# Performance work log

Hardware: AMD Instinct MI355X
Metric: run time of the kernel (lower is better)

## Reference

```python
import jax, jax.numpy as jnp
import numpy as np

N = 100_000      # nodes
E = 1_600_000    # edges
DIN = 128
DH = 128
DOUT = 2
BN_EPS = 1e-5


def setup_inputs() -> dict:
    key = jax.random.key(0)
    ks = jax.random.split(key, 14)
    s_in = 1.0 / np.sqrt(DIN)
    s_h = 1.0 / np.sqrt(DH)
    return {
        "x": jax.random.normal(ks[0], (N, DIN), jnp.float32),
        "edge_index": jax.random.randint(ks[1], (2, E), 0, N, jnp.int32),
        "W1": jax.random.normal(ks[2], (DIN, DH), jnp.float32) * s_in,
        "b1": jnp.zeros((DH,), jnp.float32),
        "W2": jax.random.normal(ks[3], (DH, DH), jnp.float32) * s_h,
        "b2": jnp.zeros((DH,), jnp.float32),
        "W3": jax.random.normal(ks[4], (DH, DH), jnp.float32) * s_h,
        "b3": jnp.zeros((DH,), jnp.float32),
        "gamma": jnp.ones((DH,), jnp.float32),
        "beta": jnp.zeros((DH,), jnp.float32),
        "Wc": jax.random.normal(ks[5], (DH, DH), jnp.float32) * s_h,
        "bc": jnp.zeros((DH,), jnp.float32),
        "Wr": jax.random.normal(ks[6], (DH, DOUT), jnp.float32) * s_h,
        "br": jnp.zeros((DOUT,), jnp.float32),
    }


def reference(x, edge_index, W1, b1, W2, b2, W3, b3, gamma, beta, Wc, bc, Wr, br):
    src, dst = edge_index[0], edge_index[1]
    # GCN symmetric normalization with self-loops (deg includes self-loop)
    deg = jnp.zeros((N,), x.dtype).at[dst].add(1.0) + 1.0
    dinv = jax.lax.rsqrt(deg)
    coef = (dinv[src] * dinv[dst])[:, None]        # [E,1]
    self_coef = (dinv * dinv)[:, None]             # [N,1] self-loop weight

    def gcn_conv(h, W, b):
        h = h @ W                                  # [N,DH] dense transform
        agg = jnp.zeros((N, h.shape[1]), h.dtype).at[dst].add(h[src] * coef)
        return agg + h * self_coef + b

    h = jax.nn.relu(gcn_conv(x, W1, b1))
    h = jax.nn.relu(gcn_conv(h, W2, b2))   # dropout is identity at inference
    h = jax.nn.relu(gcn_conv(h, W3, b3))
    # BatchNorm1d over the node dimension (training-mode batch statistics)
    mu = h.mean(axis=0)
    var = h.var(axis=0)
    h = (h - mu) * jax.lax.rsqrt(var + BN_EPS) * gamma + beta
    h = jax.nn.relu(h @ Wc + bc)
    return h @ Wr + br
```

## Files before the change

kernel.cpp:

```cpp
#include <hip/hip_runtime.h>

#define DHC 128
#define BSHIFT 8
#define BSIZE 256

typedef __attribute__((ext_vector_type(8))) __bf16 bf16x8;
typedef __attribute__((ext_vector_type(8))) unsigned short ushort8;
typedef __attribute__((ext_vector_type(4))) float floatx4;

__device__ inline unsigned short f2bf(float f) {
    unsigned int u = __float_as_uint(f);
    return (unsigned short)((u + 0x7FFFu + ((u >> 16) & 1u)) >> 16);
}
__device__ inline float bf2f_lo(unsigned int v) { return __uint_as_float(v << 16); }
__device__ inline float bf2f_hi(unsigned int v) { return __uint_as_float(v & 0xFFFF0000u); }


__global__ __launch_bounds__(256) void bucket_hist(const int* __restrict__ dst,
                                                   int* __restrict__ bcount, int e) {
    __shared__ int h[512];
    for (int i = threadIdx.x; i < 512; i += 256) h[i] = 0;
    __syncthreads();
    int base = blockIdx.x * 4096 + threadIdx.x;
#pragma unroll
    for (int j = 0; j < 16; j++) {
        int i = base + j * 256;
        if (i < e) atomicAdd(&h[dst[i] >> BSHIFT], 1);
    }
    __syncthreads();
    for (int i = threadIdx.x; i < 512; i += 256)
        if (h[i]) atomicAdd(&bcount[i], h[i]);
}

__global__ void bucket_scan(const int* __restrict__ bcount, int* __restrict__ bbase,
                            int* __restrict__ bcur, int nb, int e) {
    __shared__ int s[512];
    int t = threadIdx.x;
    s[t] = (t < nb) ? bcount[t] : 0;
    __syncthreads();
    for (int off = 1; off < 512; off <<= 1) {
        int add = (t >= off) ? s[t - off] : 0;
        __syncthreads();
        s[t] += add;
        __syncthreads();
    }
    if (t < nb) {
        int ex = (t == 0) ? 0 : s[t - 1];
        bbase[t] = ex;
        bcur[t] = ex;
    }
    if (t == 0) bbase[nb] = e;
}

__global__ __launch_bounds__(256) void bucket_scatter(const int* __restrict__ src,
                                                      const int* __restrict__ dst,
                                                      int* __restrict__ bcur,
                                                      unsigned int* __restrict__ ebuf, int e) {
    __shared__ int h[512];
    __shared__ int rsv[512];
    for (int i = threadIdx.x; i < 512; i += 256) h[i] = 0;
    __syncthreads();
    int base = blockIdx.x * 4096 + threadIdx.x;
    int sreg[16], dreg[16];
#pragma unroll
    for (int j = 0; j < 16; j++) {
        int i = base + j * 256;
        if (i < e) {
            sreg[j] = src[i];
            dreg[j] = dst[i];
            atomicAdd(&h[dreg[j] >> BSHIFT], 1);
        } else {
            dreg[j] = -1;
        }
    }
    __syncthreads();
    for (int i = threadIdx.x; i < 512; i += 256) {
        int c = h[i];
        rsv[i] = c ? atomicAdd(&bcur[i], c) : 0;
        h[i] = 0;
    }
    __syncthreads();
#pragma unroll
    for (int j = 0; j < 16; j++) {
        if (dreg[j] >= 0) {
            int b = dreg[j] >> BSHIFT;
            int pos = rsv[b] + atomicAdd(&h[b], 1);
            ebuf[pos] = (unsigned int)sreg[j] | ((unsigned int)(dreg[j] & (BSIZE - 1)) << 20);
        }
    }
}

__global__ __launch_bounds__(256) void bucket_dega(const unsigned int* __restrict__ ebuf,
                                                   const int* __restrict__ bbase,
                                                   int* __restrict__ degs,
                                                   int* __restrict__ pbsum,
                                                   float* __restrict__ dinv, int n) {
    __shared__ int ldeg[256];
    __shared__ int red[256];
    int b = blockIdx.x, t = threadIdx.x;
    int beg = bbase[b], end = bbase[b + 1];
    ldeg[t] = 0;
    __syncthreads();
    for (int i = beg + t; i < end; i += 256) atomicAdd(&ldeg[ebuf[i] >> 20], 1);
    __syncthreads();
    int node = (b << BSHIFT) + t;
    int deg = ldeg[t];
    int pdeg = (deg + 7) & ~7;
    if (node < n) {
        degs[node] = deg;
        dinv[node] = rsqrtf((float)(deg + 1));
    } else {
        pdeg = 0;
    }
    red[t] = pdeg;
    __syncthreads();
    for (int off = 128; off > 0; off >>= 1) {
        if (t < off) red[t] += red[t + off];
        __syncthreads();
    }
    if (t == 0) pbsum[b] = red[0];
}

__global__ void pscan(const int* __restrict__ pbsum, int* __restrict__ pbase,
                      int* __restrict__ row_ptr, int nb, int n) {
    __shared__ int s[512];
    int t = threadIdx.x;
    s[t] = (t < nb) ? pbsum[t] : 0;
    __syncthreads();
    for (int off = 1; off < 512; off <<= 1) {
        int add = (t >= off) ? s[t - off] : 0;
        __syncthreads();
        s[t] += add;
        __syncthreads();
    }
    if (t < nb) pbase[t] = (t == 0) ? 0 : s[t - 1];
    if (t == 0) {
        pbase[nb] = s[nb - 1];
        row_ptr[n] = s[nb - 1];
    }
}

__global__ __launch_bounds__(256) void bucket_csr(const unsigned int* __restrict__ ebuf,
                                                  const int* __restrict__ bbase,
                                                  const int* __restrict__ pbase,
                                                  const int* __restrict__ degs,
                                                  int* __restrict__ row_ptr,
                                                  int* __restrict__ csr, int n) {
    __shared__ int lcur[256];
    __shared__ int lscan[256];
    int b = blockIdx.x, t = threadIdx.x;
    int beg = bbase[b], end = bbase[b + 1];
    int node = (b << BSHIFT) + t;
    int deg = (node < n) ? degs[node] : 0;
    int pdeg = (deg + 7) & ~7;
    lscan[t] = pdeg;
    __syncthreads();
    for (int off = 1; off < 256; off <<= 1) {
        int add = (t >= off) ? lscan[t - off] : 0;
        __syncthreads();
        lscan[t] += add;
        __syncthreads();
    }
    int rp = pbase[b] + lscan[t] - pdeg;
    if (node < n) row_ptr[node] = rp;
    lcur[t] = rp;
    __syncthreads();
    for (int i = beg + t; i < end; i += 256) {
        unsigned int p = ebuf[i];
        int pos = atomicAdd(&lcur[p >> 20], 1);
        csr[pos] = (int)(p & 0xFFFFFu);
    }
    __syncthreads();
    for (int j = deg; j < pdeg; j++) csr[rp + j] = n;
}

__global__ void wconv3_k(const float* __restrict__ W1, const float* __restrict__ W2,
                         const float* __restrict__ W3, unsigned short* __restrict__ WTall,
                         unsigned short* __restrict__ dumA, unsigned short* __restrict__ dumB) {
    if (blockIdx.x == 0 && threadIdx.x < 128) {
        dumA[threadIdx.x] = 0;
        dumB[threadIdx.x] = 0;
    }
    int idx = blockIdx.x * 256 + threadIdx.x;
    int wsel = idx >> 14;
    int i = idx & 16383;
    int nn = i >> 7, k = i & 127;
    const float* W = (wsel == 0) ? W1 : (wsel == 1) ? W2 : W3;
    WTall[idx] = f2bf(W[k * 128 + nn]);
}

template <int MODE, int AF32>
__global__ __launch_bounds__(256, 4) void gemm_k(const void* __restrict__ Avoid,
                                                 const unsigned short* __restrict__ WT,
                                                 const float* __restrict__ bias,
                                                 unsigned short* __restrict__ outB,
                                                 float* __restrict__ outF,
                                                 const float* __restrict__ Wr,
                                                 const float* __restrict__ br,
                                                 const float* __restrict__ dinvp, int n) {
    __shared__ unsigned short Ws[32 * 512];
    {
        for (int c = threadIdx.x; c < 2048; c += 256) {
            int f = c >> 6;
            int l = c & 63;
            int ks = f >> 3, ct = f & 7;
            int nn = ct * 16 + (l & 15);
            int kb = ks * 32 + (l >> 4) * 8;
            *(uint4*)(&Ws[c * 8]) = *(const uint4*)(&WT[nn * 128 + kb]);
        }
    }
    __syncthreads();
    const int wave = threadIdx.x >> 6;
    const int lane = threadIdx.x & 63;
    const int rowbase = blockIdx.x * 128 + wave * 32;
    const int m = lane & 15;
    const int kq = lane >> 4;

    floatx4 acc[2][8];
#pragma unroll
    for (int rt = 0; rt < 2; rt++)
#pragma unroll
        for (int ct = 0; ct < 8; ct++) acc[rt][ct] = (floatx4){0.f, 0.f, 0.f, 0.f};

    const int r0 = min(rowbase + m, n - 1);
    const int r1 = min(rowbase + 16 + m, n - 1);

#pragma unroll
    for (int ks = 0; ks < 4; ks++) {
        const int kb = ks * 32 + kq * 8;
        bf16x8 a0, a1;
        if (AF32) {
            const float* Af = (const float*)Avoid;
            float4 f00 = *(const float4*)(Af + (size_t)r0 * 128 + kb);
            float4 f01 = *(const float4*)(Af + (size_t)r0 * 128 + kb + 4);
            float4 f10 = *(const float4*)(Af + (size_t)r1 * 128 + kb);
            float4 f11 = *(const float4*)(Af + (size_t)r1 * 128 + kb + 4);
            ushort8 u0, u1;
            u0[0] = f2bf(f00.x); u0[1] = f2bf(f00.y); u0[2] = f2bf(f00.z); u0[3] = f2bf(f00.w);
            u0[4] = f2bf(f01.x); u0[5] = f2bf(f01.y); u0[6] = f2bf(f01.z); u0[7] = f2bf(f01.w);
            u1[0] = f2bf(f10.x); u1[1] = f2bf(f10.y); u1[2] = f2bf(f10.z); u1[3] = f2bf(f10.w);
            u1[4] = f2bf(f11.x); u1[5] = f2bf(f11.y); u1[6] = f2bf(f11.z); u1[7] = f2bf(f11.w);
            a0 = __builtin_bit_cast(bf16x8, u0);
            a1 = __builtin_bit_cast(bf16x8, u1);
        } else {
            const unsigned short* Ab = (const unsigned short*)Avoid;
            a0 = __builtin_bit_cast(bf16x8, *(const ushort8*)(Ab + (size_t)r0 * 128 + kb));
            a1 = __builtin_bit_cast(bf16x8, *(const ushort8*)(Ab + (size_t)r1 * 128 + kb));
        }
#pragma unroll
        for (int ct = 0; ct < 8; ct++) {
            bf16x8 bfr = __builtin_bit_cast(bf16x8,
                *(const ushort8*)(&Ws[(ks * 8 + ct) * 512 + lane * 8]));
            acc[0][ct] = __builtin_amdgcn_mfma_f32_16x16x32_bf16(a0, bfr, acc[0][ct], 0, 0, 0);
            acc[1][ct] = __builtin_amdgcn_mfma_f32_16x16x32_bf16(a1, bfr, acc[1][ct], 0, 0, 0);
        }
    }

    if (MODE == 0) {
#pragma unroll
        for (int rt = 0; rt < 2; rt++) {
#pragma unroll
            for (int i = 0; i < 4; i++) {
                int r = rowbase + rt * 16 + kq * 4 + i;
                if (r < n) {
                    float dv = dinvp[r];
#pragma unroll
                    for (int ct = 0; ct < 8; ct++) {
                        int col = ct * 16 + m;
                        outB[(size_t)r * 128 + col] = f2bf(acc[rt][ct][i] * dv);
                    }
                }
            }
        }
    } else {
        float bcv[8], wr0[8], wr1[8];
#pragma unroll
        for (int ct = 0; ct < 8; ct++) {
            int col = ct * 16 + m;
            bcv[ct] = bias[col];
            float2 wv = ((const float2*)Wr)[col];
            wr0[ct] = wv.x;
            wr1[ct] = wv.y;
        }
        float br0 = br[0], br1 = br[1];
#pragma unroll
        for (int rt = 0; rt < 2; rt++) {
#pragma unroll
            for (int i = 0; i < 4; i++) {
                float p0 = 0.f, p1 = 0.f;
#pragma unroll
                for (int ct = 0; ct < 8; ct++) {
                    float v = fmaxf(acc[rt][ct][i] + bcv[ct], 0.f);
                    p0 = fmaf(v, wr0[ct], p0);
                    p1 = fmaf(v, wr1[ct], p1);
                }
#pragma unroll
                for (int mk = 1; mk < 16; mk <<= 1) {
                    p0 += __shfl_xor(p0, mk);
                    p1 += __shfl_xor(p1, mk);
                }
                int r = rowbase + rt * 16 + kq * 4 + i;
                if (m == 0 && r < n) ((float2*)outF)[r] = make_float2(p0 + br0, p1 + br1);
            }
        }
    }
}

#define ACC8(v)                                          \
    a[0] += bf2f_lo((v).x); a[1] += bf2f_hi((v).x);      \
    a[2] += bf2f_lo((v).y); a[3] += bf2f_hi((v).y);      \
    a[4] += bf2f_lo((v).z); a[5] += bf2f_hi((v).z);      \
    a[6] += bf2f_lo((v).w); a[7] += bf2f_hi((v).w);

__global__ __launch_bounds__(256) void agg_k(const unsigned short* __restrict__ hS,
                                             const int* __restrict__ csr,
                                             const int* __restrict__ row_ptr,
                                             const float* __restrict__ dinv,
                                             const float* __restrict__ bias,
                                             unsigned short* __restrict__ out, int n) {
    int node = blockIdx.x * 16 + (threadIdx.x >> 4);
    int t = threadIdx.x & 15;
    if (node >= n) return;
    const uint4* h4 = (const uint4*)hS;
    uint4 vs = h4[(size_t)node * 16 + t];
    int beg = row_ptr[node], pend = row_ptr[node + 1];
    float dd = dinv[node];

    float a[8];
    a[0] = bf2f_lo(vs.x); a[1] = bf2f_hi(vs.x);
    a[2] = bf2f_lo(vs.y); a[3] = bf2f_hi(vs.y);
    a[4] = bf2f_lo(vs.z); a[5] = bf2f_hi(vs.z);
    a[6] = bf2f_lo(vs.w); a[7] = bf2f_hi(vs.w);

    const int4* cp = (const int4*)(csr + beg);
    int nc = (pend - beg) >> 3;
    if (nc > 0) {
        int4 i0 = cp[0], i1 = cp[1];
        for (int k = 0; k < nc; k++) {
            uint4 v0 = h4[(size_t)(unsigned)i0.x * 16 + t];
            uint4 v1 = h4[(size_t)(unsigned)i0.y * 16 + t];
            uint4 v2 = h4[(size_t)(unsigned)i0.z * 16 + t];
            uint4 v3 = h4[(size_t)(unsigned)i0.w * 16 + t];
            uint4 v4 = h4[(size_t)(unsigned)i1.x * 16 + t];
            uint4 v5 = h4[(size_t)(unsigned)i1.y * 16 + t];
            uint4 v6 = h4[(size_t)(unsigned)i1.z * 16 + t];
            uint4 v7 = h4[(size_t)(unsigned)i1.w * 16 + t];
            int4 p0 = cp[2 * k + 2];
            int4 p1 = cp[2 * k + 3];
            ACC8(v0); ACC8(v1); ACC8(v2); ACC8(v3);
            ACC8(v4); ACC8(v5); ACC8(v6); ACC8(v7);
            i0 = p0; i1 = p1;
        }
    }

    float4 b0 = ((const float4*)bias)[t * 2];
    float4 b1 = ((const float4*)bias)[t * 2 + 1];
    uint4 o;
    o.x = (unsigned int)f2bf(fmaxf(fmaf(dd, a[0], b0.x), 0.f)) |
          ((unsigned int)f2bf(fmaxf(fmaf(dd, a[1], b0.y), 0.f)) << 16);
    o.y = (unsigned int)f2bf(fmaxf(fmaf(dd, a[2], b0.z), 0.f)) |
          ((unsigned int)f2bf(fmaxf(fmaf(dd, a[3], b0.w), 0.f)) << 16);
    o.z = (unsigned int)f2bf(fmaxf(fmaf(dd, a[4], b1.x), 0.f)) |
          ((unsigned int)f2bf(fmaxf(fmaf(dd, a[5], b1.y), 0.f)) << 16);
    o.w = (unsigned int)f2bf(fmaxf(fmaf(dd, a[6], b1.z), 0.f)) |
          ((unsigned int)f2bf(fmaxf(fmaf(dd, a[7], b1.w), 0.f)) << 16);
    ((uint4*)out)[(size_t)node * 16 + t] = o;
}

__global__ __launch_bounds__(256) void bn_stats(const unsigned short* __restrict__ h,
                                                float* __restrict__ gsum,
                                                float* __restrict__ gsumsq, int n) {
    __shared__ float red[4][256];
    int l = threadIdx.x & 63;
    int rs = threadIdx.x >> 6;
    float s0 = 0.f, s1 = 0.f, q0 = 0.f, q1 = 0.f;
    for (int r = blockIdx.x * 4 + rs; r < n; r += gridDim.x * 4) {
        unsigned int v = *(const unsigned int*)(h + (size_t)r * 128 + l * 2);
        float a = bf2f_lo(v), b = bf2f_hi(v);
        s0 += a;
        s1 += b;
        q0 = fmaf(a, a, q0);
        q1 = fmaf(b, b, q1);
    }
    red[0][threadIdx.x] = s0;
    red[1][threadIdx.x] = s1;
    red[2][threadIdx.x] = q0;
    red[3][threadIdx.x] = q1;
    __syncthreads();
    if (threadIdx.x < 64) {
        float S0 = 0.f, S1 = 0.f, Q0 = 0.f, Q1 = 0.f;
#pragma unroll
        for (int j = 0; j < 4; j++) {
            S0 += red[0][j * 64 + l];
            S1 += red[1][j * 64 + l];
            Q0 += red[2][j * 64 + l];
            Q1 += red[3][j * 64 + l];
        }
        atomicAdd(&gsum[2 * l + 0], S0);
        atomicAdd(&gsum[2 * l + 1], S1);
        atomicAdd(&gsumsq[2 * l + 0], Q0);
        atomicAdd(&gsumsq[2 * l + 1], Q1);
    }
}

__global__ void bn_finalize(const float* __restrict__ gsum, const float* __restrict__ gsumsq,
                            const float* __restrict__ gamma, const float* __restrict__ beta,
                            const float* __restrict__ bc, float* __restrict__ scale,
                            float* __restrict__ shift, float* __restrict__ bcP, float invN) {
    int j = threadIdx.x;
    float mu = gsum[j] * invN;
    float var = gsumsq[j] * invN - mu * mu;
    float sc = gamma[j] * rsqrtf(var + 1e-5f);
    scale[j] = sc;
    shift[j] = beta[j] - mu * sc;
    bcP[j] = bc[j];
}

__global__ __launch_bounds__(256) void wcfold(const float* __restrict__ Wc,
                                              const float* __restrict__ scale,
                                              const float* __restrict__ shift,
                                              unsigned short* __restrict__ WcT,
                                              float* __restrict__ bcP) {
    __shared__ float scS[128], shS[128];
    if (threadIdx.x < 128) {
        scS[threadIdx.x] = scale[threadIdx.x];
        shS[threadIdx.x] = shift[threadIdx.x];
    }
    __syncthreads();
    int idx = blockIdx.x * 256 + threadIdx.x;
    int j = idx & 127, k = idx >> 7;
    float w = Wc[k * 128 + j];
    WcT[j * 128 + k] = f2bf(scS[k] * w);
    atomicAdd(&bcP[j], shS[k] * w);
}


extern "C" void kernel_launch(void* const* d_in, const int* in_sizes, int n_in,
                              void* d_out, int out_size, void* d_ws, size_t ws_size,
                              hipStream_t stream) {
    const float* x = (const float*)d_in[0];
    const int* ei = (const int*)d_in[1];
    const float* W1 = (const float*)d_in[2];
    const float* b1 = (const float*)d_in[3];
    const float* W2 = (const float*)d_in[4];
    const float* b2 = (const float*)d_in[5];
    const float* W3 = (const float*)d_in[6];
    const float* b3 = (const float*)d_in[7];
    const float* gamma = (const float*)d_in[8];
    const float* beta = (const float*)d_in[9];
    const float* Wc = (const float*)d_in[10];
    const float* bc = (const float*)d_in[11];
    const float* Wr = (const float*)d_in[12];
    const float* br = (const float*)d_in[13];
    float* out = (float*)d_out;

    const int N = in_sizes[0] / DHC;
    const int E = in_sizes[1] / 2;
    const int* srcIdx = ei;
    const int* dstIdx = ei + E;
    const int NB = (N + BSIZE - 1) >> BSHIFT;

    char* w = (char*)d_ws;
    size_t off = 0;
    auto alloc = [&](size_t bytes) -> void* {
        void* p = w + off;
        off += (bytes + 255) & ~(size_t)255;
        return p;
    };
    unsigned short* bufA = (unsigned short*)alloc((size_t)(N + 1) * DHC * 2);
    unsigned short* bufB = (unsigned short*)alloc((size_t)(N + 1) * DHC * 2);
    unsigned int* ebuf = (unsigned int*)alloc((size_t)E * 4);
    int* csr_src = (int*)alloc(((size_t)E + 8 * (size_t)N + 16) * 4);
    int* row_ptr = (int*)alloc((size_t)(N + 1) * 4);
    float* dinv = (float*)alloc((size_t)N * 4);
    int* degs = (int*)alloc((size_t)N * 4);
    int* bcount = (int*)alloc(512 * 4 + 256 * 4);
    float* stats = (float*)(bcount + 512);
    float* gsum = stats;
    float* gsumsq = stats + 128;
    int* bbase = (int*)alloc(513 * 4);
    int* bcur = (int*)alloc(512 * 4);
    int* pbsum = (int*)alloc(512 * 4);
    int* pbase = (int*)alloc(513 * 4);
    unsigned short* WTall = (unsigned short*)alloc((size_t)3 * 16384 * 2);
    unsigned short* WT1 = WTall;
    unsigned short* WT2 = WTall + 16384;
    unsigned short* WT3 = WTall + 32768;
    unsigned short* WcT = (unsigned short*)alloc(16384 * 2);
    float* scale = (float*)alloc(128 * 4);
    float* shift = (float*)alloc(128 * 4);
    float* bcP = (float*)alloc(128 * 4);
    (void)ws_size; (void)n_in; (void)out_size;

    hipMemsetAsync(bcount, 0, 512 * 4 + 256 * 4, stream);

    const int EB = (E + 4095) / 4096;
    bucket_hist<<<EB, 256, 0, stream>>>(dstIdx, bcount, E);
    bucket_scan<<<1, 512, 0, stream>>>(bcount, bbase, bcur, NB, E);
    bucket_scatter<<<EB, 256, 0, stream>>>(srcIdx, dstIdx, bcur, ebuf, E);
    bucket_dega<<<NB, 256, 0, stream>>>(ebuf, bbase, degs, pbsum, dinv, N);
    pscan<<<1, 512, 0, stream>>>(pbsum, pbase, row_ptr, NB, N);
    bucket_csr<<<NB, 256, 0, stream>>>(ebuf, bbase, pbase, degs, row_ptr, csr_src, N);

    wconv3_k<<<192, 256, 0, stream>>>(W1, W2, W3, WTall,
                                      bufA + (size_t)N * DHC, bufB + (size_t)N * DHC);

    const int gemmBlocks = (N + 127) / 128;
    const int aggBlocks = (N + 15) / 16;

    gemm_k<0, 1><<<gemmBlocks, 256, 0, stream>>>(x, WT1, nullptr, bufB, nullptr, nullptr, nullptr, dinv, N);
    agg_k<<<aggBlocks, 256, 0, stream>>>(bufB, csr_src, row_ptr, dinv, b1, bufA, N);
    gemm_k<0, 0><<<gemmBlocks, 256, 0, stream>>>(bufA, WT2, nullptr, bufB, nullptr, nullptr, nullptr, dinv, N);
    agg_k<<<aggBlocks, 256, 0, stream>>>(bufB, csr_src, row_ptr, dinv, b2, bufA, N);
    gemm_k<0, 0><<<gemmBlocks, 256, 0, stream>>>(bufA, WT3, nullptr, bufB, nullptr, nullptr, nullptr, dinv, N);
    agg_k<<<aggBlocks, 256, 0, stream>>>(bufB, csr_src, row_ptr, dinv, b3, bufA, N);

    bn_stats<<<256, 256, 0, stream>>>(bufA, gsum, gsumsq, N);
    bn_finalize<<<1, 128, 0, stream>>>(gsum, gsumsq, gamma, beta, bc, scale, shift, bcP, 1.0f / (float)N);
    wcfold<<<64, 256, 0, stream>>>(Wc, scale, shift, WcT, bcP);
    gemm_k<2, 0><<<gemmBlocks, 256, 0, stream>>>(bufA, WcT, bcP, nullptr, out, Wr, br, dinv, N);
}
```

Measured before the change: 449.9 us.

## Split aggregation into feature halves and fuse BN statistics into last aggregation

The aggregation kernel now processes one 64-feature half per launch, with 8 threads per node and 32 nodes per block, and is launched twice per layer. Each launch gathers half as many bytes per neighbor row, which shrinks the working set so gathered rows are more likely to hit in L2/MALL. The last layer's aggregation also accumulates BatchNorm sums and sums of squares through shuffles, shared atomics and global atomics, removing the separate bn_stats pass. The costs are that CSR indices and row pointers are read twice per layer and there are extra launches.

```diff
diff --git a/kernel.cpp b/kernel.cpp
--- a/kernel.cpp
+++ b/kernel.cpp
@@ -312,39 +312,56 @@
     a[4] += bf2f_lo((v).z); a[5] += bf2f_hi((v).z);      \
     a[6] += bf2f_lo((v).w); a[7] += bf2f_hi((v).w);
 
+template <int HALF, int STATS>
 __global__ __launch_bounds__(256) void agg_k(const unsigned short* __restrict__ hS,
                                              const int* __restrict__ csr,
                                              const int* __restrict__ row_ptr,
                                              const float* __restrict__ dinv,
                                              const float* __restrict__ bias,
-                                             unsigned short* __restrict__ out, int n) {
-    int node = blockIdx.x * 16 + (threadIdx.x >> 4);
-    int t = threadIdx.x & 15;
-    if (node >= n) return;
+                                             unsigned short* __restrict__ out,
+                                             float* __restrict__ gsum,
+                                             float* __restrict__ gsumsq, int n) {
+    __shared__ float sred[128];
+    int node = blockIdx.x * 32 + (threadIdx.x >> 3);
+    int t = threadIdx.x & 7;
+    bool valid = node < n;
+    if (!STATS && !valid) return;
+    if (STATS) {
+        if (threadIdx.x < 128) sred[threadIdx.x] = 0.f;
+        __syncthreads();
+    }
+    const int HO = HALF * 8;
     const uint4* h4 = (const uint4*)hS;
-    uint4 vs = h4[(size_t)node * 16 + t];
-    int beg = row_ptr[node], pend = row_ptr[node + 1];
-    float dd = dinv[node];
 
     float a[8];
-    a[0] = bf2f_lo(vs.x); a[1] = bf2f_hi(vs.x);
-    a[2] = bf2f_lo(vs.y); a[3] = bf2f_hi(vs.y);
-    a[4] = bf2f_lo(vs.z); a[5] = bf2f_hi(vs.z);
-    a[6] = bf2f_lo(vs.w); a[7] = bf2f_hi(vs.w);
+#pragma unroll
+    for (int j = 0; j < 8; j++) a[j] = 0.f;
+    float dd = 0.f;
+    int beg = 0, pend = 0;
+    if (valid) {
+        uint4 vs = h4[(size_t)node * 16 + HO + t];
+        beg = row_ptr[node];
+        pend = row_ptr[node + 1];
+        dd = dinv[node];
+        a[0] = bf2f_lo(vs.x); a[1] = bf2f_hi(vs.x);
+        a[2] = bf2f_lo(vs.y); a[3] = bf2f_hi(vs.y);
+        a[4] = bf2f_lo(vs.z); a[5] = bf2f_hi(vs.z);
+        a[6] = bf2f_lo(vs.w); a[7] = bf2f_hi(vs.w);
+    }
 
     const int4* cp = (const int4*)(csr + beg);
     int nc = (pend - beg) >> 3;
     if (nc > 0) {
         int4 i0 = cp[0], i1 = cp[1];
         for (int k = 0; k < nc; k++) {
-            uint4 v0 = h4[(size_t)(unsigned)i0.x * 16 + t];
-            uint4 v1 = h4[(size_t)(unsigned)i0.y * 16 + t];
-            uint4 v2 = h4[(size_t)(unsigned)i0.z * 16 + t];
-            uint4 v3 = h4[(size_t)(unsigned)i0.w * 16 + t];
-            uint4 v4 = h4[(size_t)(unsigned)i1.x * 16 + t];
-            uint4 v5 = h4[(size_t)(unsigned)i1.y * 16 + t];
-            uint4 v6 = h4[(size_t)(unsigned)i1.z * 16 + t];
-            uint4 v7 = h4[(size_t)(unsigned)i1.w * 16 + t];
+            uint4 v0 = h4[(size_t)(unsigned)i0.x * 16 + HO + t];
+            uint4 v1 = h4[(size_t)(unsigned)i0.y * 16 + HO + t];
+            uint4 v2 = h4[(size_t)(unsigned)i0.z * 16 + HO + t];
+            uint4 v3 = h4[(size_t)(unsigned)i0.w * 16 + HO + t];
+            uint4 v4 = h4[(size_t)(unsigned)i1.x * 16 + HO + t];
+            uint4 v5 = h4[(size_t)(unsigned)i1.y * 16 + HO + t];
+            uint4 v6 = h4[(size_t)(unsigned)i1.z * 16 + HO + t];
+            uint4 v7 = h4[(size_t)(unsigned)i1.w * 16 + HO + t];
             int4 p0 = cp[2 * k + 2];
             int4 p1 = cp[2 * k + 3];
             ACC8(v0); ACC8(v1); ACC8(v2); ACC8(v3);
@@ -353,53 +370,46 @@
         }
     }
 
-    float4 b0 = ((const float4*)bias)[t * 2];
-    float4 b1 = ((const float4*)bias)[t * 2 + 1];
-    uint4 o;
-    o.x = (unsigned int)f2bf(fmaxf(fmaf(dd, a[0], b0.x), 0.f)) |
-          ((unsigned int)f2bf(fmaxf(fmaf(dd, a[1], b0.y), 0.f)) << 16);
-    o.y = (unsigned int)f2bf(fmaxf(fmaf(dd, a[2], b0.z), 0.f)) |
-          ((unsigned int)f2bf(fmaxf(fmaf(dd, a[3], b0.w), 0.f)) << 16);
-    o.z = (unsigned int)f2bf(fmaxf(fmaf(dd, a[4], b1.x), 0.f)) |
-          ((unsigned int)f2bf(fmaxf(fmaf(dd, a[5], b1.y), 0.f)) << 16);
-    o.w = (unsigned int)f2bf(fmaxf(fmaf(dd, a[6], b1.z), 0.f)) |
-          ((unsigned int)f2bf(fmaxf(fmaf(dd, a[7], b1.w), 0.f)) << 16);
-    ((uint4*)out)[(size_t)node * 16 + t] = o;
-}
-
-__global__ __launch_bounds__(256) void bn_stats(const unsigned short* __restrict__ h,
-                                                float* __restrict__ gsum,
-                                                float* __restrict__ gsumsq, int n) {
-    __shared__ float red[4][256];
-    int l = threadIdx.x & 63;
-    int rs = threadIdx.x >> 6;
-    float s0 = 0.f, s1 = 0.f, q0 = 0.f, q1 = 0.f;
-    for (int r = blockIdx.x * 4 + rs; r < n; r += gridDim.x * 4) {
-        unsigned int v = *(const unsigned int*)(h + (size_t)r * 128 + l * 2);
-        float a = bf2f_lo(v), b = bf2f_hi(v);
-        s0 += a;
-        s1 += b;
-        q0 = fmaf(a, a, q0);
-        q1 = fmaf(b, b, q1);
-    }
-    red[0][threadIdx.x] = s0;
-    red[1][threadIdx.x] = s1;
-    red[2][threadIdx.x] = q0;
-    red[3][threadIdx.x] = q1;
-    __syncthreads();
-    if (threadIdx.x < 64) {
-        float S0 = 0.f, S1 = 0.f, Q0 = 0.f, Q1 = 0.f;
-#pragma unroll
-        for (int j = 0; j < 4; j++) {
-            S0 += red[0][j * 64 + l];
-            S1 += red[1][j * 64 + l];
-            Q0 += red[2][j * 64 + l];
-            Q1 += red[3][j * 64 + l];
-        }
-        atomicAdd(&gsum[2 * l + 0], S0);
-        atomicAdd(&gsum[2 * l + 1], S1);
-        atomicAdd(&gsumsq[2 * l + 0], Q0);
-        atomicAdd(&gsumsq[2 * l + 1], Q1);
+    float vout[8];
+    if (valid) {
+        float4 b0 = ((const float4*)bias)[HALF * 16 + t * 2];
+        float4 b1 = ((const float4*)bias)[HALF * 16 + t * 2 + 1];
+        vout[0] = fmaxf(fmaf(dd, a[0], b0.x), 0.f);
+        vout[1] = fmaxf(fmaf(dd, a[1], b0.y), 0.f);
+        vout[2] = fmaxf(fmaf(dd, a[2], b0.z), 0.f);
+        vout[3] = fmaxf(fmaf(dd, a[3], b0.w), 0.f);
+        vout[4] = fmaxf(fmaf(dd, a[4], b1.x), 0.f);
+        vout[5] = fmaxf(fmaf(dd, a[5], b1.y), 0.f);
+        vout[6] = fmaxf(fmaf(dd, a[6], b1.z), 0.f);
+        vout[7] = fmaxf(fmaf(dd, a[7], b1.w), 0.f);
+        uint4 o;
+        o.x = (unsigned int)f2bf(vout[0]) | ((unsigned int)f2bf(vout[1]) << 16);
+        o.y = (unsigned int)f2bf(vout[2]) | ((unsigned int)f2bf(vout[3]) << 16);
+        o.z = (unsigned int)f2bf(vout[4]) | ((unsigned int)f2bf(vout[5]) << 16);
+        o.w = (unsigned int)f2bf(vout[6]) | ((unsigned int)f2bf(vout[7]) << 16);
+        ((uint4*)out)[(size_t)node * 16 + HO + t] = o;
+    } else {
+#pragma unroll
+        for (int j = 0; j < 8; j++) vout[j] = 0.f;
+    }
+
+    if (STATS) {
+#pragma unroll
+        for (int j = 0; j < 8; j++) {
+            float sv = vout[j], qv = vout[j] * vout[j];
+            sv += __shfl_xor(sv, 8);  qv += __shfl_xor(qv, 8);
+            sv += __shfl_xor(sv, 16); qv += __shfl_xor(qv, 16);
+            sv += __shfl_xor(sv, 32); qv += __shfl_xor(qv, 32);
+            if ((threadIdx.x & 63) < 8) {
+                atomicAdd(&sred[t * 8 + j], sv);
+                atomicAdd(&sred[64 + t * 8 + j], qv);
+            }
+        }
+        __syncthreads();
+        if (threadIdx.x < 64)
+            atomicAdd(&gsum[HALF * 64 + threadIdx.x], sred[threadIdx.x]);
+        else if (threadIdx.x < 128)
+            atomicAdd(&gsumsq[HALF * 64 + (threadIdx.x - 64)], sred[threadIdx.x]);
     }
 }
 
@@ -506,16 +516,18 @@
                                       bufA + (size_t)N * DHC, bufB + (size_t)N * DHC);
 
     const int gemmBlocks = (N + 127) / 128;
-    const int aggBlocks = (N + 15) / 16;
+    const int aggBlocks = (N + 31) / 32;
 
     gemm_k<0, 1><<<gemmBlocks, 256, 0, stream>>>(x, WT1, nullptr, bufB, nullptr, nullptr, nullptr, dinv, N);
-    agg_k<<<aggBlocks, 256, 0, stream>>>(bufB, csr_src, row_ptr, dinv, b1, bufA, N);
+    agg_k<0, 0><<<aggBlocks, 256, 0, stream>>>(bufB, csr_src, row_ptr, dinv, b1, bufA, nullptr, nullptr, N);
+    agg_k<1, 0><<<aggBlocks, 256, 0, stream>>>(bufB, csr_src, row_ptr, dinv, b1, bufA, nullptr, nullptr, N);
     gemm_k<0, 0><<<gemmBlocks, 256, 0, stream>>>(bufA, WT2, nullptr, bufB, nullptr, nullptr, nullptr, dinv, N);
-    agg_k<<<aggBlocks, 256, 0, stream>>>(bufB, csr_src, row_ptr, dinv, b2, bufA, N);
+    agg_k<0, 0><<<aggBlocks, 256, 0, stream>>>(bufB, csr_src, row_ptr, dinv, b2, bufA, nullptr, nullptr, N);
+    agg_k<1, 0><<<aggBlocks, 256, 0, stream>>>(bufB, csr_src, row_ptr, dinv, b2, bufA, nullptr, nullptr, N);
     gemm_k<0, 0><<<gemmBlocks, 256, 0, stream>>>(bufA, WT3, nullptr, bufB, nullptr, nullptr, nullptr, dinv, N);
-    agg_k<<<aggBlocks, 256, 0, stream>>>(bufB, csr_src, row_ptr, dinv, b3, bufA, N);
-
-    bn_stats<<<256, 256, 0, stream>>>(bufA, gsum, gsumsq, N);
+    agg_k<0, 1><<<aggBlocks, 256, 0, stream>>>(bufB, csr_src, row_ptr, dinv, b3, bufA, gsum, gsumsq, N);
+    agg_k<1, 1><<<aggBlocks, 256, 0, stream>>>(bufB, csr_src, row_ptr, dinv, b3, bufA, gsum, gsumsq, N);
+
     bn_finalize<<<1, 128, 0, stream>>>(gsum, gsumsq, gamma, beta, bc, scale, shift, bcP, 1.0f / (float)N);
     wcfold<<<64, 256, 0, stream>>>(Wc, scale, shift, WcT, bcP);
     gemm_k<2, 0><<<gemmBlocks, 256, 0, stream>>>(bufA, WcT, bcP, nullptr, out, Wr, br, dinv, N);
```

Measured after the change: 533.1 us. 1.19x slower.
